# Performance work log

Hardware: AMD Instinct MI355X
Metric: run time of the kernel (lower is better)

The kernel has to match this reference:

```python
import jax, jax.numpy as jnp
import numpy as np
from jax.scipy.special import erf

# Module hyperparameters (from init_kwargs)
IN_C, OUT_C = 256, 512
IN_S, OUT_S = 196, 49
C_DIM, S_DIM = 512, 196        # lcm(256,512), lcm(196,49)
IN_CF, OUT_CF = 2, 1           # channel factors
IN_SF, OUT_SF = 1, 4           # spatio factors
NUM_POINTS = 5
NUM_STEPS = 3
STEP = 0.33333
BATCH = 256

# manet.func.sigmoid surrogates (all map R -> (0,1))
def ngd(x):   # normal gaussian distribution CDF
    return 0.5 * (1.0 + erf(x * 0.7071067811865476))

def nerf(x):  # normalized erf
    return 0.5 * (1.0 + erf(x))

def alg1(x):  # algebraic sigmoid, order 1
    return 0.5 * (x / (1.0 + jnp.abs(x))) + 0.5


def setup_inputs() -> dict:
    key = jax.random.key(0)
    ks = jax.random.split(key, 5)
    data = jax.random.normal(ks[0], (BATCH, IN_C, IN_S), dtype=jnp.float32)
    in_weight = jax.random.normal(ks[1], (1, C_DIM, S_DIM), dtype=jnp.float32)
    in_bias = jax.random.normal(ks[2], (1, C_DIM, S_DIM), dtype=jnp.float32)
    out_weight = jax.random.normal(ks[3], (1, C_DIM, S_DIM), dtype=jnp.float32)
    out_bias = jax.random.normal(ks[4], (1, C_DIM, S_DIM), dtype=jnp.float32)
    angles = jnp.linspace(0.0, 2.0 * np.pi, NUM_POINTS).astype(jnp.float32)
    velocity = jnp.linspace(0.0, 1.0, NUM_POINTS).astype(jnp.float32)
    return {"data": data, "in_weight": in_weight, "in_bias": in_bias,
            "out_weight": out_weight, "out_bias": out_bias,
            "angles": angles, "velocity": velocity}


def _clamped_bgn(index):
    # faithful reproduction of accessor() clamping arithmetic
    bgn = jnp.floor(index).astype(jnp.int32)
    bgn = bgn * (bgn >= 0)
    bgn = bgn * (bgn <= NUM_POINTS - 2) + (bgn - 1) * (bgn > NUM_POINTS - 2)
    bgn = bgn * (bgn <= NUM_POINTS - 2) + (bgn - 1) * (bgn > NUM_POINTS - 2)
    return bgn


def _access(memory, x, sig_fn):
    # data-dependent piecewise-linear LUT lookup
    index = sig_fn(x) * NUM_POINTS
    bgn = _clamped_bgn(index)
    pos = index - bgn
    return (1.0 - pos) * memory[bgn] + pos * memory[bgn + 1]


def reference(data, in_weight, in_bias, out_weight, out_bias, angles, velocity):
    # expansion: [B, Cin, Sin] -> [B, C_DIM, S_DIM]
    x = data.reshape(-1, IN_C, 1, IN_S, 1)
    x = x * in_weight.reshape(1, IN_C, IN_CF, IN_S, IN_SF)
    x = x + in_bias.reshape(1, IN_C, IN_CF, IN_S, IN_SF)
    x = x.reshape(-1, C_DIM, S_DIM)

    # nonlinear: iterative MAC step; note step() itself multiplies by STEP,
    # and nonlinear() multiplies the step output by STEP again -> STEP*STEP.
    for _ in range(NUM_STEPS):
        ang = _access(angles, x, ngd)
        vel = _access(velocity, x, nerf)
        x = x + (vel * jnp.cos(ang) + x * vel * jnp.sin(ang)) * (STEP * STEP)

    # attention gate
    att = alg1(x * out_weight + out_bias)
    x = x * att

    # reduction: [B, C_DIM, S_DIM] -> [B, OUT_C, OUT_S]
    x = x.reshape(-1, OUT_CF, OUT_C, OUT_SF, OUT_S)
    return jnp.sum(x, axis=(1, 3))
```

## Files before the change

### kernel.cpp

```cpp
#include <hip/hip_runtime.h>
#include <hip/hip_fp16.h>


#define STEP2f    0.11110889f
#define INV_2PI   0.15915494309189535f
#define LOG2E     1.4426950408889634f
#define LUT_N     4096
#define LUT_B     8.0f
#define LUT_SCALE 256.0f
#define BPT       4

struct MacCoef {
    float ca1, ca3, cb1, cb3;
    float A0r, dAr;
    float V0s, dVs;
};

__device__ __forceinline__ MacCoef make_coef(const float* angles, const float* velocity) {
    MacCoef c;
    c.ca1 = -1.5957691216f * LOG2E;
    c.ca3 = -0.0713548168f * LOG2E;
    c.cb1 = c.ca1 * 1.41421356237f;
    c.cb3 = c.ca3 * 2.82842712475f;
    c.A0r = angles[0] * INV_2PI;
    c.dAr = (angles[4] - angles[0]) * 1.25f * INV_2PI;
    c.V0s = velocity[0] * STEP2f;
    c.dVs = (velocity[4] - velocity[0]) * 1.25f * STEP2f;
    return c;
}

__device__ __forceinline__ float mac_step(float x, const MacCoef& c) {
    float xx = x * x;
    float ua = fminf(x * fmaf(c.ca3, xx, c.ca1), 60.0f);
    float ub = fminf(x * fmaf(c.cb3, xx, c.cb1), 60.0f);
    float ea = __builtin_amdgcn_exp2f(ua);
    float eb = __builtin_amdgcn_exp2f(ub);
    float da = 1.0f + ea, db = 1.0f + eb;
    float rp = __builtin_amdgcn_rcpf(da * db);
    float sa = db * rp;
    float sb = da * rp;
    float r  = fmaf(c.dAr, sa, c.A0r);
    float v2 = fmaf(c.dVs, sb, c.V0s);
    float sn = __builtin_amdgcn_sinf(r);
    float cs = __builtin_amdgcn_cosf(r);
    return fmaf(v2, fmaf(x, sn, cs), x);
}

__device__ __forceinline__ float F3(float x, const MacCoef& c) {
    x = mac_step(x, c);
    x = mac_step(x, c);
    return mac_step(x, c);
}

__global__ __launch_bounds__(256) void build_lut(
    const float* __restrict__ angles, const float* __restrict__ velocity,
    __half2* __restrict__ lut2)
{
    int i = blockIdx.x * 256 + threadIdx.x;
    if (i >= LUT_N) return;
    MacCoef c = make_coef(angles, velocity);
    float x0 = fmaf((float)i,       1.0f / LUT_SCALE, -LUT_B);
    float x1 = fmaf((float)(i + 1), 1.0f / LUT_SCALE, -LUT_B);
    lut2[i] = __halves2half2(__float2half(F3(x0, c)), __float2half(F3(x1, c)));
}

__global__ __launch_bounds__(256, 8) void mac_kernel(
    const float* __restrict__ data,
    const float* __restrict__ in_w,
    const float* __restrict__ in_b,
    const float* __restrict__ out_w,
    const float* __restrict__ out_b,
    const float* __restrict__ angles,
    const float* __restrict__ velocity,
    const __half2* __restrict__ glut,
    float* __restrict__ out)
{
    __shared__ __half2 lut[LUT_N];

    const int tid = threadIdx.x;
    {
        const uint4* src = (const uint4*)glut;
        uint4* dst = (uint4*)lut;
#pragma unroll
        for (int i = 0; i < 4; ++i) dst[tid + 256 * i] = src[tid + 256 * i];
    }

    const int t  = blockIdx.x * 256 + tid;
    const int os = t % 49;
    const int c  = t / 49;

    MacCoef mc = make_coef(angles, velocity);
    float snp = __builtin_amdgcn_sinf(mc.A0r + mc.dAr);
    float cP  = fmaf(mc.V0s + mc.dVs, snp, 1.0f);
    float slopeP = cP * cP * cP;
    float snn = __builtin_amdgcn_sinf(mc.A0r);
    float cN  = fmaf(mc.V0s, snn, 1.0f);
    float slopeN = cN * cN * cN;

    float iw[2][4], ib[2][4], ow[2][4], ob[2][4];
    const int wb = c * 392 + os;
#pragma unroll
    for (int e = 0; e < 2; ++e)
#pragma unroll
        for (int sf = 0; sf < 4; ++sf) {
            int s = wb + e * 196 + sf * 49;
            iw[e][sf] = in_w[s];  ib[e][sf] = in_b[s];
            ow[e][sf] = out_w[s]; ob[e][sf] = out_b[s];
        }

    __syncthreads();

    const float* dptr = data + ((size_t)(blockIdx.y * BPT) * 256 + c) * 196 + os;
    float*       optr = out  + (size_t)(blockIdx.y * BPT) * 25088 + c * 98 + os;

    float r0[4], r1[4], r2[4];
#pragma unroll
    for (int sf = 0; sf < 4; ++sf) r0[sf] = dptr[sf * 49];
#pragma unroll
    for (int sf = 0; sf < 4; ++sf) r1[sf] = dptr[50176 + sf * 49];

#pragma unroll
    for (int k = 0; k < BPT; ++k) {
        if (k + 2 < BPT) {
            const float* dn = dptr + (size_t)(k + 2) * 50176;
#pragma unroll
            for (int sf = 0; sf < 4; ++sf) r2[sf] = dn[sf * 49];
        }

        float yv[2][4], tg[2][4];
#pragma unroll
        for (int sf = 0; sf < 4; ++sf) {
            float xv = r0[sf];
#pragma unroll
            for (int e = 0; e < 2; ++e) {
                float x0 = fmaf(xv, iw[e][sf], ib[e][sf]);
                float xc = fminf(fmaxf(x0, -LUT_B), LUT_B);
                float fi = fmaf(xc, LUT_SCALE, 2048.0f);
                int   j  = min((int)fi, LUT_N - 1);
                float fr = fi - (float)j;
                __half2 p = lut[j];
                float lo = __low2float(p), hi = __high2float(p);
                float v  = fmaf(fr, hi - lo, lo);
                float dd = x0 - xc;
                float sl = x0 > 0.0f ? slopeP : slopeN;
                float y  = fmaf(dd, sl, v);
                yv[e][sf] = y;
                tg[e][sf] = fmaf(y, ow[e][sf], ob[e][sf]);
            }
        }

#pragma unroll
        for (int e = 0; e < 2; ++e) {
            float acc = 0.0f;
#pragma unroll
            for (int p = 0; p < 2; ++p) {
                float t0 = tg[e][2 * p], t1 = tg[e][2 * p + 1];
                float d0 = 1.0f + fabsf(t0);
                float d1 = 1.0f + fabsf(t1);
                float rr = __builtin_amdgcn_rcpf(d0 * d1);
                acc = fmaf(yv[e][2 * p],     fmaf(0.5f * t0, d1 * rr, 0.5f), acc);
                acc = fmaf(yv[e][2 * p + 1], fmaf(0.5f * t1, d0 * rr, 0.5f), acc);
            }
            optr[(size_t)k * 25088 + e * 49] = acc;
        }

#pragma unroll
        for (int sf = 0; sf < 4; ++sf) { r0[sf] = r1[sf]; r1[sf] = r2[sf]; }
    }
}

extern "C" void kernel_launch(void* const* d_in, const int* in_sizes, int n_in,
                              void* d_out, int out_size, void* d_ws, size_t ws_size,
                              hipStream_t stream) {
    const float* data   = (const float*)d_in[0];
    const float* in_w   = (const float*)d_in[1];
    const float* in_b   = (const float*)d_in[2];
    const float* out_w  = (const float*)d_in[3];
    const float* out_b  = (const float*)d_in[4];
    const float* angles = (const float*)d_in[5];
    const float* vel    = (const float*)d_in[6];
    float* out = (float*)d_out;
    __half2* lut = (__half2*)d_ws;

    build_lut<<<dim3(LUT_N / 256), 256, 0, stream>>>(angles, vel, lut);

    dim3 grid(49, 256 / BPT);
    mac_kernel<<<grid, 256, 0, stream>>>(data, in_w, in_b, out_w, out_b,
                                         angles, vel, lut, out);
}
```

Baseline: 118.5 us.

## Fuse LUT build into main kernel with coarser LUT and batched prefetch

Drops the separate build_lut launch. Each block now builds a smaller 1024-entry half2 LUT in shared memory itself, at a coarser 1/64 spacing, overlapping that work with global loads of the data. Blocks shrink to 128 threads and each handles 16 batches in two chunks of 8, with the whole chunk's inputs loaded up front. This removes a kernel launch and the workspace round trip but repeats the LUT computation in every block. The coarser LUT also lowers interpolation accuracy, and the larger register arrays may reduce occupancy.

```diff
diff --git a/kernel.cpp b/kernel.cpp
--- a/kernel.cpp
+++ b/kernel.cpp
@@ -5,10 +5,13 @@
 #define STEP2f    0.11110889f
 #define INV_2PI   0.15915494309189535f
 #define LOG2E     1.4426950408889634f
-#define LUT_N     4096
+#define LUT_N     1024
 #define LUT_B     8.0f
-#define LUT_SCALE 256.0f
-#define BPT       4
+#define LUT_SCALE 64.0f
+#define LUT_BIAS  512.0f
+#define BPT       8
+#define NCHUNK    2
+#define TPB       128
 
 struct MacCoef {
     float ca1, ca3, cb1, cb3;
@@ -52,90 +55,23 @@
     return mac_step(x, c);
 }
 
-__global__ __launch_bounds__(256) void build_lut(
-    const float* __restrict__ angles, const float* __restrict__ velocity,
-    __half2* __restrict__ lut2)
+__device__ __forceinline__ void compute_chunk(
+    const float rb[BPT][4],
+    const float iw[2][4], const float ib[2][4],
+    const float ow[2][4], const float ob[2][4],
+    float slopeP, float slopeN, const __half2* lut, float* optr)
 {
-    int i = blockIdx.x * 256 + threadIdx.x;
-    if (i >= LUT_N) return;
-    MacCoef c = make_coef(angles, velocity);
-    float x0 = fmaf((float)i,       1.0f / LUT_SCALE, -LUT_B);
-    float x1 = fmaf((float)(i + 1), 1.0f / LUT_SCALE, -LUT_B);
-    lut2[i] = __halves2half2(__float2half(F3(x0, c)), __float2half(F3(x1, c)));
-}
-
-__global__ __launch_bounds__(256, 8) void mac_kernel(
-    const float* __restrict__ data,
-    const float* __restrict__ in_w,
-    const float* __restrict__ in_b,
-    const float* __restrict__ out_w,
-    const float* __restrict__ out_b,
-    const float* __restrict__ angles,
-    const float* __restrict__ velocity,
-    const __half2* __restrict__ glut,
-    float* __restrict__ out)
-{
-    __shared__ __half2 lut[LUT_N];
-
-    const int tid = threadIdx.x;
-    {
-        const uint4* src = (const uint4*)glut;
-        uint4* dst = (uint4*)lut;
-#pragma unroll
-        for (int i = 0; i < 4; ++i) dst[tid + 256 * i] = src[tid + 256 * i];
-    }
-
-    const int t  = blockIdx.x * 256 + tid;
-    const int os = t % 49;
-    const int c  = t / 49;
-
-    MacCoef mc = make_coef(angles, velocity);
-    float snp = __builtin_amdgcn_sinf(mc.A0r + mc.dAr);
-    float cP  = fmaf(mc.V0s + mc.dVs, snp, 1.0f);
-    float slopeP = cP * cP * cP;
-    float snn = __builtin_amdgcn_sinf(mc.A0r);
-    float cN  = fmaf(mc.V0s, snn, 1.0f);
-    float slopeN = cN * cN * cN;
-
-    float iw[2][4], ib[2][4], ow[2][4], ob[2][4];
-    const int wb = c * 392 + os;
-#pragma unroll
-    for (int e = 0; e < 2; ++e)
-#pragma unroll
-        for (int sf = 0; sf < 4; ++sf) {
-            int s = wb + e * 196 + sf * 49;
-            iw[e][sf] = in_w[s];  ib[e][sf] = in_b[s];
-            ow[e][sf] = out_w[s]; ob[e][sf] = out_b[s];
-        }
-
-    __syncthreads();
-
-    const float* dptr = data + ((size_t)(blockIdx.y * BPT) * 256 + c) * 196 + os;
-    float*       optr = out  + (size_t)(blockIdx.y * BPT) * 25088 + c * 98 + os;
-
-    float r0[4], r1[4], r2[4];
-#pragma unroll
-    for (int sf = 0; sf < 4; ++sf) r0[sf] = dptr[sf * 49];
-#pragma unroll
-    for (int sf = 0; sf < 4; ++sf) r1[sf] = dptr[50176 + sf * 49];
-
 #pragma unroll
     for (int k = 0; k < BPT; ++k) {
-        if (k + 2 < BPT) {
-            const float* dn = dptr + (size_t)(k + 2) * 50176;
-#pragma unroll
-            for (int sf = 0; sf < 4; ++sf) r2[sf] = dn[sf * 49];
-        }
-
         float yv[2][4], tg[2][4];
 #pragma unroll
         for (int sf = 0; sf < 4; ++sf) {
-            float xv = r0[sf];
+            float xv = rb[k][sf];
 #pragma unroll
             for (int e = 0; e < 2; ++e) {
                 float x0 = fmaf(xv, iw[e][sf], ib[e][sf]);
                 float xc = fminf(fmaxf(x0, -LUT_B), LUT_B);
-                float fi = fmaf(xc, LUT_SCALE, 2048.0f);
+                float fi = fmaf(xc, LUT_SCALE, LUT_BIAS);
                 int   j  = min((int)fi, LUT_N - 1);
                 float fr = fi - (float)j;
                 __half2 p = lut[j];
@@ -163,10 +99,84 @@
             }
             optr[(size_t)k * 25088 + e * 49] = acc;
         }
+    }
+}
+
+__global__ __launch_bounds__(TPB, 3) void mac_kernel(
+    const float* __restrict__ data,
+    const float* __restrict__ in_w,
+    const float* __restrict__ in_b,
+    const float* __restrict__ out_w,
+    const float* __restrict__ out_b,
+    const float* __restrict__ angles,
+    const float* __restrict__ velocity,
+    float* __restrict__ out)
+{
+    __shared__ __half2 lut[LUT_N];
+
+    const int tid = threadIdx.x;
+    const int t  = blockIdx.x * TPB + tid;
+    const int os = t % 49;
+    const int c  = t / 49;
+
+    const float* dptr = data + ((size_t)(blockIdx.y * BPT * NCHUNK) * 256 + c) * 196 + os;
+    float*       optr = out  + (size_t)(blockIdx.y * BPT * NCHUNK) * 25088 + c * 98 + os;
+
+    float rb0[BPT][4], rb1[BPT][4];
+#pragma unroll
+    for (int k = 0; k < BPT; ++k)
+#pragma unroll
+        for (int sf = 0; sf < 4; ++sf) rb0[k][sf] = dptr[(size_t)k * 50176 + sf * 49];
+
+    float iw[2][4], ibv[2][4], ow[2][4], obv[2][4];
+    {
+        const int wb = c * 392 + os;
+#pragma unroll
+        for (int e = 0; e < 2; ++e)
+#pragma unroll
+            for (int sf = 0; sf < 4; ++sf) {
+                int s = wb + e * 196 + sf * 49;
+                iw[e][sf] = in_w[s];  ibv[e][sf] = in_b[s];
+                ow[e][sf] = out_w[s]; obv[e][sf] = out_b[s];
+            }
+    }
+
+    MacCoef mc = make_coef(angles, velocity);
+    float snp = __builtin_amdgcn_sinf(mc.A0r + mc.dAr);
+    float cP  = fmaf(mc.V0s + mc.dVs, snp, 1.0f);
+    float slopeP = cP * cP * cP;
+    float snn = __builtin_amdgcn_sinf(mc.A0r);
+    float cN  = fmaf(mc.V0s, snn, 1.0f);
+    float slopeN = cN * cN * cN;
+
+    {
+        uint4* dst = (uint4*)lut;
+#pragma unroll
+        for (int g = 0; g < 2; ++g) {
+            const int base = g * (LUT_N / 2) + 4 * tid;
+            float f[5];
+#pragma unroll
+            for (int n = 0; n < 5; ++n)
+                f[n] = F3(fmaf((float)(base + n), 1.0f / LUT_SCALE, -LUT_B), mc);
+            union { __half2 h[4]; uint4 u; } pk;
+#pragma unroll
+            for (int n = 0; n < 4; ++n)
+                pk.h[n] = __halves2half2(__float2half(f[n]), __float2half(f[n + 1]));
+            dst[tid + g * TPB] = pk.u;
+        }
+    }
+
+    __syncthreads();
 
 #pragma unroll
-        for (int sf = 0; sf < 4; ++sf) { r0[sf] = r1[sf]; r1[sf] = r2[sf]; }
-    }
+    for (int k = 0; k < BPT; ++k)
+#pragma unroll
+        for (int sf = 0; sf < 4; ++sf)
+            rb1[k][sf] = dptr[(size_t)(BPT + k) * 50176 + sf * 49];
+
+    compute_chunk(rb0, iw, ibv, ow, obv, slopeP, slopeN, lut, optr);
+    compute_chunk(rb1, iw, ibv, ow, obv, slopeP, slopeN, lut,
+                  optr + (size_t)BPT * 25088);
 }
 
 extern "C" void kernel_launch(void* const* d_in, const int* in_sizes, int n_in,
@@ -180,11 +190,9 @@
     const float* angles = (const float*)d_in[5];
     const float* vel    = (const float*)d_in[6];
     float* out = (float*)d_out;
-    __half2* lut = (__half2*)d_ws;
+    (void)d_ws; (void)ws_size;
 
-    build_lut<<<dim3(LUT_N / 256), 256, 0, stream>>>(angles, vel, lut);
-
-    dim3 grid(49, 256 / BPT);
-    mac_kernel<<<grid, 256, 0, stream>>>(data, in_w, in_b, out_w, out_b,
-                                         angles, vel, lut, out);
+    dim3 grid(12544 / TPB, 256 / (BPT * NCHUNK));
+    mac_kernel<<<grid, TPB, 0, stream>>>(data, in_w, in_b, out_w, out_b,
+                                         angles, vel, out);
 }
```

Result: no change. 119.4 us (+0.8%).
